# Optimization experiments

Hardware: AMD Instinct MI355X
Metric: run time of the kernel (lower is better)

Reference implementation:

```python
import jax, jax.numpy as jnp
import numpy as np


def setup_inputs() -> dict:
    key = jax.random.key(0)
    k1, k2 = jax.random.split(key)
    B, L, J, N = 8, 32, 128, 512
    ypred = jax.random.normal(k1, (B, L, J, N), dtype=jnp.float32)
    xyz = jax.random.normal(k2, (B, L, N, 3), dtype=jnp.float32)
    return {"ypred": ypred, "xyz": xyz}


def _pairwise_dist(x):
    # x: [BL, N, 3] -> Euclidean distance [BL, N, N] via the mm trick,
    # with the diagonal forced to exactly 0 (matching torch.cdist(x, x)).
    sq = jnp.sum(x * x, axis=-1)                       # [BL, N]
    d2 = sq[:, :, None] + sq[:, None, :] - 2.0 * jnp.einsum('bnd,bmd->bnm', x, x)
    d2 = jnp.maximum(d2, 0.0)
    dist = jnp.sqrt(d2)
    n = x.shape[1]
    eye = jnp.eye(n, dtype=bool)
    return jnp.where(eye[None, :, :], 0.0, dist)


def reference(ypred, xyz):
    B, L, J, N = ypred.shape
    x = xyz.reshape(B * L, N, 3)
    dist = _pairwise_dist(x)                           # [BL, N, N]
    max_idx = jnp.argmax(dist, axis=2)                 # [BL, N] farthest point
    dist_masked = jnp.where(dist == 0.0, 1e6, dist)    # mask self (and exact dupes)
    min_idx = jnp.argmin(dist_masked, axis=2)          # [BL, N] nearest point

    # per-point logit vectors: [BL, N, J]
    yp = jnp.transpose(ypred, (0, 1, 3, 2)).reshape(B * L, N, J)
    sim = jnp.einsum('bnj,bmj->bnm', yp, yp)           # [BL, N, N]

    sim_at_max = jnp.take_along_axis(sim, max_idx[:, :, None], axis=2)[..., 0]
    sim_at_min = jnp.take_along_axis(sim, min_idx[:, :, None], axis=2)[..., 0]
    return jnp.mean(sim_at_max - sim_at_min)
```

## Files before the change

### kernel.cpp

```cpp
#include <hip/hip_runtime.h>

#pragma clang fp contract(off)

#define NBATCH 256
#define NPTS   512
#define JDIM   128
#define NPAIR  (NBATCH * NPTS)

__global__ __launch_bounds__(128) void argmm_kernel(
    const float* __restrict__ xyz,
    int* __restrict__ pmax,
    int* __restrict__ pmin)
{
    __shared__ float4 xyzS[NPTS];

    const int t  = threadIdx.x;
    const int bl = blockIdx.x >> 2;
    const int qq = blockIdx.x & 3;
    const float* xp = xyz + (size_t)bl * NPTS * 3;

    #pragma unroll
    for (int i = 0; i < 4; ++i) {
        int m = t + i * 128;
        float x = xp[3 * m], y = xp[3 * m + 1], z = xp[3 * m + 2];
        float sq = (x * x + y * y) + z * z;
        xyzS[m] = make_float4(-2.0f * x, -2.0f * y, -2.0f * z, sq);
    }

    const int p = qq * 128 + t;
    float ox = xp[3 * p], oy = xp[3 * p + 1], oz = xp[3 * p + 2];
    float oq = (ox * ox + oy * oy) + oz * oz;
    __syncthreads();

    float bmax = -1.0f, bmin = 3.0e38f;
    int   ima  = 0,     imi  = 0;
    #pragma unroll 8
    for (int m = 0; m < NPTS; ++m) {
        float4 qv = xyzS[m];
        float dt = (ox * qv.x + oy * qv.y) + oz * qv.z;
        float d2 = (oq + qv.w) + dt;
        bool gt = d2 > bmax;
        ima = gt ? m : ima;  bmax = gt ? d2 : bmax;
        bool lt = (d2 < bmin) && (d2 > 0.0f);
        imi = lt ? m : imi;  bmin = lt ? d2 : bmin;
    }

    pmax[bl * NPTS + p] = ima;
    pmin[bl * NPTS + p] = imi;
}

__global__ __launch_bounds__(512) void sim_kernel(
    const float* __restrict__ ypred,
    const int* __restrict__ pmax,
    const int* __restrict__ pmin,
    float* __restrict__ partials)
{
    __shared__ float L[16 * NPTS];
    __shared__ float wred[8];

    const int t  = threadIdx.x;
    const int bl = blockIdx.x >> 3;
    const int c  = blockIdx.x & 7;

    const int pma = pmax[bl * NPTS + t];
    const int pmi = pmin[bl * NPTS + t];

    const float4* src = (const float4*)(ypred + (size_t)bl * JDIM * NPTS
                                              + (size_t)c * 16 * NPTS);
    float4 v0 = src[t], v1 = src[512 + t], v2 = src[1024 + t], v3 = src[1536 + t];
    float4* dst = (float4*)L;
    dst[t] = v0;  dst[512 + t] = v1;  dst[1024 + t] = v2;  dst[1536 + t] = v3;
    __syncthreads();

    float accP = 0.0f, accM = 0.0f;
    #pragma unroll
    for (int r = 0; r < 16; ++r) {
        float a  = L[r * NPTS + t];
        float b  = L[r * NPTS + pma];
        float cm = L[r * NPTS + pmi];
        accP = fmaf(a, b, accP);
        accM = fmaf(a, cm, accM);
    }

    float d = accP - accM;
    #pragma unroll
    for (int off = 32; off > 0; off >>= 1)
        d += __shfl_down(d, off);
    if ((t & 63) == 0) wred[t >> 6] = d;
    __syncthreads();
    if (t == 0) {
        float ssum = 0.0f;
        #pragma unroll
        for (int w = 0; w < 8; ++w) ssum += wred[w];
        partials[blockIdx.x] = ssum;
    }
}

__global__ __launch_bounds__(1024) void reduce_mean_kernel(
    const float* __restrict__ partials, float* __restrict__ out)
{
    const int t = threadIdx.x;
    float v = partials[t] + partials[t + 1024];
    #pragma unroll
    for (int off = 32; off > 0; off >>= 1)
        v += __shfl_down(v, off);

    __shared__ float w[16];
    if ((t & 63) == 0) w[t >> 6] = v;
    __syncthreads();
    if (t == 0) {
        float s = 0.0f;
        #pragma unroll
        for (int i = 0; i < 16; ++i) s += w[i];
        out[0] = s * (1.0f / (float)NPAIR);
    }
}

extern "C" void kernel_launch(void* const* d_in, const int* in_sizes, int n_in,
                              void* d_out, int out_size, void* d_ws, size_t ws_size,
                              hipStream_t stream) {
    const float* ypred = (const float*)d_in[0];
    const float* xyz   = (const float*)d_in[1];

    int*   pmax     = (int*)d_ws;
    int*   pmin     = pmax + NPAIR;
    float* partials = (float*)(pmin + NPAIR);
    float* out      = (float*)d_out;

    argmm_kernel<<<4 * NBATCH, 128, 0, stream>>>(xyz, pmax, pmin);
    sim_kernel<<<8 * NBATCH, 512, 0, stream>>>(ypred, pmax, pmin, partials);
    reduce_mean_kernel<<<1, 1024, 0, stream>>>(partials, out);
}
```

Baseline: 125.4 us.

## Split argmax/argmin scan across four threads per point with shuffle merge

The distance scan now uses four threads per query point, each covering a 128-point quarter, so blocks grow from 128 to 512 threads. Partial argmax/argmin results are merged with xor shuffles that keep the lower-index winner on ties. The shared array gets one padding slot per 128 entries to spread LDS bank accesses, and the query point is read from shared memory instead of global. This raises parallelism and occupancy for the compute-bound scan, at the cost of extra shuffle work. The recovered query coordinates pass through a -2 then -0.5 scaling, which could differ from the original in the last bit.

```diff
diff --git a/kernel.cpp b/kernel.cpp
--- a/kernel.cpp
+++ b/kernel.cpp
@@ -7,46 +7,65 @@
 #define JDIM   128
 #define NPAIR  (NBATCH * NPTS)
 
-__global__ __launch_bounds__(128) void argmm_kernel(
+__global__ __launch_bounds__(512) void argmm_kernel(
     const float* __restrict__ xyz,
     int* __restrict__ pmax,
     int* __restrict__ pmin)
 {
-    __shared__ float4 xyzS[NPTS];
+    __shared__ float4 xyzS[NPTS + 4];
 
     const int t  = threadIdx.x;
     const int bl = blockIdx.x >> 2;
     const int qq = blockIdx.x & 3;
     const float* xp = xyz + (size_t)bl * NPTS * 3;
 
-    #pragma unroll
-    for (int i = 0; i < 4; ++i) {
-        int m = t + i * 128;
-        float x = xp[3 * m], y = xp[3 * m + 1], z = xp[3 * m + 2];
+    {
+        float x = xp[3 * t], y = xp[3 * t + 1], z = xp[3 * t + 2];
         float sq = (x * x + y * y) + z * z;
-        xyzS[m] = make_float4(-2.0f * x, -2.0f * y, -2.0f * z, sq);
+        xyzS[t + (t >> 7)] = make_float4(-2.0f * x, -2.0f * y, -2.0f * z, sq);
     }
-
-    const int p = qq * 128 + t;
-    float ox = xp[3 * p], oy = xp[3 * p + 1], oz = xp[3 * p + 2];
-    float oq = (ox * ox + oy * oy) + oz * oz;
     __syncthreads();
 
+    const int p = qq * 128 + (t >> 2);
+    const int q = t & 3;
+
+    float4 ov = xyzS[p + (p >> 7)];
+    float ox = -0.5f * ov.x, oy = -0.5f * ov.y, oz = -0.5f * ov.z;
+    float oq_ = ov.w;
+
+    const float4* xb = &xyzS[q];
+    const int m0 = q << 7;
     float bmax = -1.0f, bmin = 3.0e38f;
-    int   ima  = 0,     imi  = 0;
+    int   ima  = m0,    imi  = m0;
     #pragma unroll 8
-    for (int m = 0; m < NPTS; ++m) {
-        float4 qv = xyzS[m];
+    for (int mm = 0; mm < 128; ++mm) {
+        int m = m0 + mm;
+        float4 qv = xb[m];
         float dt = (ox * qv.x + oy * qv.y) + oz * qv.z;
-        float d2 = (oq + qv.w) + dt;
+        float d2 = (oq_ + qv.w) + dt;
         bool gt = d2 > bmax;
         ima = gt ? m : ima;  bmax = gt ? d2 : bmax;
         bool lt = (d2 < bmin) && (d2 > 0.0f);
         imi = lt ? m : imi;  bmin = lt ? d2 : bmin;
     }
 
-    pmax[bl * NPTS + p] = ima;
-    pmin[bl * NPTS + p] = imi;
+    #pragma unroll
+    for (int st = 1; st <= 2; st <<= 1) {
+        float obmax = __shfl_xor(bmax, st); int oima = __shfl_xor(ima, st);
+        float obmin = __shfl_xor(bmin, st); int oimi = __shfl_xor(imi, st);
+        bool hi = (t & st) != 0;
+        float lmax = hi ? obmax : bmax;  int lima = hi ? oima : ima;
+        float hmax = hi ? bmax : obmax;  int hima = hi ? ima  : oima;
+        bool w = hmax > lmax;
+        bmax = w ? hmax : lmax;  ima = w ? hima : lima;
+        float lmin = hi ? obmin : bmin;  int limi = hi ? oimi : imi;
+        float hmin = hi ? bmin : obmin;  int himi = hi ? imi  : oimi;
+        bool x2 = hmin < lmin;
+        bmin = x2 ? hmin : lmin;  imi = x2 ? himi : limi;
+    }
+
+    if (q == 0)      pmax[bl * NPTS + p] = ima;
+    else if (q == 1) pmin[bl * NPTS + p] = imi;
 }
 
 __global__ __launch_bounds__(512) void sim_kernel(
@@ -127,7 +146,7 @@
     float* partials = (float*)(pmin + NPAIR);
     float* out      = (float*)d_out;
 
-    argmm_kernel<<<4 * NBATCH, 128, 0, stream>>>(xyz, pmax, pmin);
+    argmm_kernel<<<4 * NBATCH, 512, 0, stream>>>(xyz, pmax, pmin);
     sim_kernel<<<8 * NBATCH, 512, 0, stream>>>(ypred, pmax, pmin, partials);
     reduce_mean_kernel<<<1, 1024, 0, stream>>>(partials, out);
 }
```

Result: faster. 116.8 us (-6.9%).
